# Kernel optimization log

Measured on AMD Instinct MI355X. Metric: run time of the kernel, lower is better.

Reference implementation:

```python
import jax, jax.numpy as jnp
import numpy as np

N_NODES = 100000
N_EDGES = 3200000
IN_F = 256
OUT_F = 128


def setup_inputs() -> dict:
    key = jax.random.key(0)
    k1, k2, k3, k4, k5, k6 = jax.random.split(key, 6)
    x = jax.random.normal(k1, (N_NODES, IN_F), dtype=jnp.float32)
    edge_row = jax.random.randint(k2, (N_EDGES,), 0, N_NODES, dtype=jnp.int32)
    edge_col = jax.random.randint(k3, (N_EDGES,), 0, N_NODES, dtype=jnp.int32)
    edge_val = jax.random.uniform(k4, (N_EDGES,), dtype=jnp.float32)
    # xavier_uniform with relu gain, as in reset_parameters
    gain = float(np.sqrt(2.0))
    bound = gain * float(np.sqrt(6.0 / (IN_F + OUT_F)))
    w = jax.random.uniform(k5, (IN_F, OUT_F), minval=-bound, maxval=bound, dtype=jnp.float32)
    std = 1.0 / float(np.sqrt(OUT_F))
    bias = jax.random.uniform(k6, (OUT_F,), minval=-std, maxval=std, dtype=jnp.float32)
    return {"x": x, "edge_row": edge_row, "edge_col": edge_col,
            "edge_val": edge_val, "w": w, "bias": bias}


def reference(x, edge_row, edge_col, edge_val, w, bias):
    # h = x @ w : dense feature transform [N, out]
    h = jnp.matmul(x, w)
    # spmm(adj, h): out[r] = sum_e adj_val[e] * h[c[e]] for edges e with row r
    msgs = edge_val[:, None] * h[edge_col]  # [E, out]
    agg = jax.ops.segment_sum(msgs, edge_row, num_segments=N_NODES)
    return agg + bias
```

## Files before the change

kernel.cpp:

```cpp
#include <hip/hip_runtime.h>

#define N_NODES 100000
#define N_EDGES 3200000
#define IN_F 256
#define OUT_F 128

#define NBIN 391
#define NBC  512
#define CHUNK 6272
#define GEMM_BLOCKS 782

typedef __attribute__((ext_vector_type(8))) short bf16x8;
typedef __attribute__((ext_vector_type(4))) float f32x4;

union U4BF { uint4 u; bf16x8 v; };

__device__ inline unsigned short f2bf(float f) {
    union { float f; unsigned u; } v; v.f = f;
    unsigned r = v.u + 0x7FFFu + ((v.u >> 16) & 1u);
    return (unsigned short)(r >> 16);
}
__device__ inline unsigned pk2(float a, float b) {
    return (unsigned)f2bf(a) | ((unsigned)f2bf(b) << 16);
}

__global__ __launch_bounds__(256) void conv_w_kernel(
    const float* __restrict__ w, uint4* __restrict__ wbfF)
{
    int tid = blockIdx.x * 256 + threadIdx.x;
    int ks = tid >> 9;
    int fn = (tid >> 6) & 7;
    int l  = tid & 63;
    int c  = fn * 16 + (l & 15);
    int k0 = ks * 32 + (l >> 4) * 8;
    const float* wp = w + (size_t)k0 * OUT_F + c;
    uint4 u;
    u.x = pk2(wp[0 * OUT_F], wp[1 * OUT_F]);
    u.y = pk2(wp[2 * OUT_F], wp[3 * OUT_F]);
    u.z = pk2(wp[4 * OUT_F], wp[5 * OUT_F]);
    u.w = pk2(wp[6 * OUT_F], wp[7 * OUT_F]);
    wbfF[tid] = u;
}

__global__ __launch_bounds__(256) void gemm_hist_kernel(
    const float* __restrict__ x, const uint4* __restrict__ wbfF,
    unsigned short* __restrict__ h,
    const int* __restrict__ erow, int* __restrict__ cntmat)
{
    __shared__ __align__(16) char smem[65536];
    const int t = threadIdx.x;

    if (blockIdx.x < GEMM_BLOCKS) {
        uint4* bsh = (uint4*)smem;
        const int lane = t & 63;
        const int wid  = t >> 6;
        const int brow = blockIdx.x * 128;
        const int ln   = lane & 15;
        const int kb   = lane >> 4;

#pragma unroll
        for (int i = 0; i < 16; ++i) bsh[i * 256 + t] = wbfF[i * 256 + t];

        int r0 = brow + wid * 32 + ln;
        int r1 = r0 + 16;
        const float* a0p = x + (size_t)(r0 < N_NODES ? r0 : N_NODES - 1) * IN_F;
        const float* a1p = x + (size_t)(r1 < N_NODES ? r1 : N_NODES - 1) * IN_F;

        f32x4 acc[2][8] = {};
        __syncthreads();

#pragma unroll
        for (int ks = 0; ks < 8; ++ks) {
            const int k = ks * 32 + kb * 8;
            U4BF a0, a1;
            {
                float4 p = *(const float4*)(a0p + k);
                float4 q = *(const float4*)(a0p + k + 4);
                a0.u.x = pk2(p.x, p.y); a0.u.y = pk2(p.z, p.w);
                a0.u.z = pk2(q.x, q.y); a0.u.w = pk2(q.z, q.w);
            }
            {
                float4 p = *(const float4*)(a1p + k);
                float4 q = *(const float4*)(a1p + k + 4);
                a1.u.x = pk2(p.x, p.y); a1.u.y = pk2(p.z, p.w);
                a1.u.z = pk2(q.x, q.y); a1.u.w = pk2(q.z, q.w);
            }
            U4BF b[8];
#pragma unroll
            for (int fn = 0; fn < 8; ++fn)
                b[fn].u = bsh[(ks * 8 + fn) * 64 + lane];
#pragma unroll
            for (int fn = 0; fn < 8; ++fn) {
                acc[0][fn] = __builtin_amdgcn_mfma_f32_16x16x32_bf16(
                    a0.v, b[fn].v, acc[0][fn], 0, 0, 0);
                acc[1][fn] = __builtin_amdgcn_mfma_f32_16x16x32_bf16(
                    a1.v, b[fn].v, acc[1][fn], 0, 0, 0);
            }
        }

#pragma unroll
        for (int fm = 0; fm < 2; ++fm) {
#pragma unroll
            for (int r = 0; r < 4; ++r) {
                int grow = brow + wid * 32 + fm * 16 + (lane >> 4) * 4 + r;
                if (grow < N_NODES) {
                    unsigned short* dst = h + (size_t)grow * OUT_F + ln;
#pragma unroll
                    for (int fn = 0; fn < 8; ++fn)
                        dst[fn * 16] = f2bf(acc[fm][fn][r]);
                }
            }
        }
    } else {
        int* lhist = (int*)smem;
        const int b = blockIdx.x - GEMM_BLOCKS;
        for (int i = t; i < NBIN; i += 256) lhist[i] = 0;
        __syncthreads();

        const int base = b * CHUNK;
        const int end  = min(base + CHUNK, N_EDGES);
        for (int i = base + t * 4; i < end; i += 1024) {
            int4 r = *(const int4*)(erow + i);
            atomicAdd(&lhist[r.x >> 8], 1);
            atomicAdd(&lhist[r.y >> 8], 1);
            atomicAdd(&lhist[r.z >> 8], 1);
            atomicAdd(&lhist[r.w >> 8], 1);
        }
        __syncthreads();

        int* dst = cntmat + (size_t)b * NBIN;
        for (int j = t; j < NBIN; j += 256) dst[j] = lhist[j];
    }
}

__global__ __launch_bounds__(256) void pass_b_kernel(
    const int* __restrict__ cntmat, int* __restrict__ blockbase,
    int* __restrict__ tot)
{
    __shared__ int sh[256];
    const int t = threadIdx.x;
    const int j = blockIdx.x;
    const int b0 = 2 * t, b1 = 2 * t + 1;
    int c0 = cntmat[(size_t)b0 * NBIN + j];
    int c1 = cntmat[(size_t)b1 * NBIN + j];
    int ps = c0 + c1;
    sh[t] = ps;
    __syncthreads();
    for (int off = 1; off < 256; off <<= 1) {
        int add = (t >= off) ? sh[t - off] : 0;
        __syncthreads();
        sh[t] += add;
        __syncthreads();
    }
    int excl = sh[t] - ps;
    blockbase[(size_t)b0 * NBIN + j] = excl;
    blockbase[(size_t)b1 * NBIN + j] = excl + c0;
    if (t == 255) tot[j] = sh[255];
}

__global__ __launch_bounds__(512) void pass_b2_kernel(
    const int* __restrict__ tot, int* __restrict__ bucket_base)
{
    __shared__ int sh[512];
    const int t = threadIdx.x;
    int v = (t < NBIN) ? tot[t] : 0;
    sh[t] = v;
    __syncthreads();
    for (int off = 1; off < 512; off <<= 1) {
        int add = (t >= off) ? sh[t - off] : 0;
        __syncthreads();
        sh[t] += add;
        __syncthreads();
    }
    if (t < NBIN + 1) bucket_base[t] = sh[t] - v;
}

__global__ __launch_bounds__(256) void pass_c_kernel(
    const int* __restrict__ erow, const int* __restrict__ ecol,
    const float* __restrict__ eval_, const int* __restrict__ blockbase,
    const int* __restrict__ bucket_base, int2* __restrict__ tmp)
{
    __shared__ int cur[NBIN];
    const int t = threadIdx.x;
    const int b = blockIdx.x;
    for (int j = t; j < NBIN; j += 256)
        cur[j] = bucket_base[j] + blockbase[(size_t)b * NBIN + j];
    __syncthreads();

    const int base = b * CHUNK;
    const int end  = min(base + CHUNK, N_EDGES);
    for (int i = base + t * 4; i < end; i += 1024) {
        int4   r = *(const int4*)(erow + i);
        int4   c = *(const int4*)(ecol + i);
        float4 v = *(const float4*)(eval_ + i);
        int p0 = atomicAdd(&cur[r.x >> 8], 1);
        tmp[p0] = make_int2(c.x | ((r.x & 255) << 17), __float_as_int(v.x));
        int p1 = atomicAdd(&cur[r.y >> 8], 1);
        tmp[p1] = make_int2(c.y | ((r.y & 255) << 17), __float_as_int(v.y));
        int p2 = atomicAdd(&cur[r.z >> 8], 1);
        tmp[p2] = make_int2(c.z | ((r.z & 255) << 17), __float_as_int(v.z));
        int p3 = atomicAdd(&cur[r.w >> 8], 1);
        tmp[p3] = make_int2(c.w | ((r.w & 255) << 17), __float_as_int(v.w));
    }
}

__global__ __launch_bounds__(256) void pass_d_kernel(
    const int2* __restrict__ tmp, const int* __restrict__ bucket_base,
    int2* __restrict__ packed, int* __restrict__ row_start,
    int* __restrict__ rowtot)
{
    __shared__ int hist[256];
    __shared__ int cursor[256];
    const int t = threadIdx.x;
    const int j = blockIdx.x;
    const int base = bucket_base[j];
    const int end  = bucket_base[j + 1];

    hist[t] = 0;
    __syncthreads();

    for (int i = base + t; i < end; i += 256)
        atomicAdd(&hist[tmp[i].x >> 17], 1);
    __syncthreads();

    int hv = hist[t];
    cursor[t] = hv;
    __syncthreads();
    for (int off = 1; off < 256; off <<= 1) {
        int add = (t >= off) ? cursor[t - off] : 0;
        __syncthreads();
        cursor[t] += add;
        __syncthreads();
    }
    int excl = cursor[t] - hv;

    int r = j * 256 + t;
    if (r < N_NODES) {
        row_start[r] = base + excl;
        rowtot[r]    = hv;
    }
    __syncthreads();
    cursor[t] = excl;
    __syncthreads();

    for (int i = base + t; i < end; i += 256) {
        int2 p = tmp[i];
        int rl = p.x >> 17;
        int pos = atomicAdd(&cursor[rl], 1);
        packed[base + pos] = make_int2(p.x & 0x1FFFF, p.y);
    }
}

__global__ __launch_bounds__(256) void aggregate_kernel(
    const int2* __restrict__ packed, const int* __restrict__ row_start,
    const int* __restrict__ rowtot, const unsigned* __restrict__ h2,
    const float* __restrict__ bias, float* __restrict__ out)
{
    int wave = (blockIdx.x * 256 + threadIdx.x) >> 6;
    int lane = threadIdx.x & 63;
    if (wave >= N_NODES) return;

    int start = __builtin_amdgcn_readfirstlane(row_start[wave]);
    int deg   = __builtin_amdgcn_readfirstlane(rowtot[wave]);
    int end   = start + deg;

    const unsigned* hb = h2 + lane;
    float ax = 0.f, ay = 0.f;

    int e = start;
    for (; e + 7 < end; e += 8) {
        int2 p0 = packed[e];
        int2 p1 = packed[e + 1];
        int2 p2 = packed[e + 2];
        int2 p3 = packed[e + 3];
        int2 p4 = packed[e + 4];
        int2 p5 = packed[e + 5];
        int2 p6 = packed[e + 6];
        int2 p7 = packed[e + 7];
        unsigned u0 = hb[(size_t)p0.x << 6];
        unsigned u1 = hb[(size_t)p1.x << 6];
        unsigned u2 = hb[(size_t)p2.x << 6];
        unsigned u3 = hb[(size_t)p3.x << 6];
        unsigned u4 = hb[(size_t)p4.x << 6];
        unsigned u5 = hb[(size_t)p5.x << 6];
        unsigned u6 = hb[(size_t)p6.x << 6];
        unsigned u7 = hb[(size_t)p7.x << 6];
        float v0 = __int_as_float(p0.y), v1 = __int_as_float(p1.y);
        float v2 = __int_as_float(p2.y), v3 = __int_as_float(p3.y);
        float v4 = __int_as_float(p4.y), v5 = __int_as_float(p5.y);
        float v6 = __int_as_float(p6.y), v7 = __int_as_float(p7.y);
        ax = fmaf(v0, __uint_as_float(u0 << 16), ax);
        ay = fmaf(v0, __uint_as_float(u0 & 0xFFFF0000u), ay);
        ax = fmaf(v1, __uint_as_float(u1 << 16), ax);
        ay = fmaf(v1, __uint_as_float(u1 & 0xFFFF0000u), ay);
        ax = fmaf(v2, __uint_as_float(u2 << 16), ax);
        ay = fmaf(v2, __uint_as_float(u2 & 0xFFFF0000u), ay);
        ax = fmaf(v3, __uint_as_float(u3 << 16), ax);
        ay = fmaf(v3, __uint_as_float(u3 & 0xFFFF0000u), ay);
        ax = fmaf(v4, __uint_as_float(u4 << 16), ax);
        ay = fmaf(v4, __uint_as_float(u4 & 0xFFFF0000u), ay);
        ax = fmaf(v5, __uint_as_float(u5 << 16), ax);
        ay = fmaf(v5, __uint_as_float(u5 & 0xFFFF0000u), ay);
        ax = fmaf(v6, __uint_as_float(u6 << 16), ax);
        ay = fmaf(v6, __uint_as_float(u6 & 0xFFFF0000u), ay);
        ax = fmaf(v7, __uint_as_float(u7 << 16), ax);
        ay = fmaf(v7, __uint_as_float(u7 & 0xFFFF0000u), ay);
    }
    for (; e < end; ++e) {
        int2 p0 = packed[e];
        unsigned u0 = hb[(size_t)p0.x << 6];
        float v0 = __int_as_float(p0.y);
        ax = fmaf(v0, __uint_as_float(u0 << 16), ax);
        ay = fmaf(v0, __uint_as_float(u0 & 0xFFFF0000u), ay);
    }

    float2 b = *(const float2*)(bias + lane * 2);
    *(float2*)(out + (size_t)wave * OUT_F + lane * 2) = make_float2(ax + b.x, ay + b.y);
}

extern "C" void kernel_launch(void* const* d_in, const int* in_sizes, int n_in,
                              void* d_out, int out_size, void* d_ws, size_t ws_size,
                              hipStream_t stream)
{
    const float* x     = (const float*)d_in[0];
    const int*   erow  = (const int*)d_in[1];
    const int*   ecol  = (const int*)d_in[2];
    const float* eval_ = (const float*)d_in[3];
    const float* w     = (const float*)d_in[4];
    const float* bias  = (const float*)d_in[5];
    float*       out   = (float*)d_out;

    char* ws = (char*)d_ws;
    unsigned short* h           = (unsigned short*)(ws);
    int2*           tmp         = (int2*)(ws + 25600000);
    int2*           packed      = (int2*)(ws + 51200000);
    int*            cntmat      = (int*)(ws + 76800000);
    int*            blockbase   = (int*)(ws + 77600768);
    int*            tot         = (int*)(ws + 78401536);
    int*            bucket_base = (int*)(ws + 78403104);
    int*            row_start   = (int*)(ws + 78404672);
    int*            rowtot      = (int*)(ws + 78804672);
    uint4*          wbfF        = (uint4*)(ws + 79204672);

    hipLaunchKernelGGL(conv_w_kernel, dim3(16), dim3(256), 0, stream, w, wbfF);

    hipLaunchKernelGGL(gemm_hist_kernel, dim3(GEMM_BLOCKS + NBC), dim3(256), 0, stream,
                       x, wbfF, h, erow, cntmat);

    hipLaunchKernelGGL(pass_b_kernel, dim3(NBIN), dim3(256), 0, stream,
                       cntmat, blockbase, tot);
    hipLaunchKernelGGL(pass_b2_kernel, dim3(1), dim3(512), 0, stream, tot, bucket_base);

    hipLaunchKernelGGL(pass_c_kernel, dim3(NBC), dim3(256), 0, stream,
                       erow, ecol, eval_, blockbase, bucket_base, tmp);

    hipLaunchKernelGGL(pass_d_kernel, dim3(NBIN), dim3(256), 0, stream,
                       tmp, bucket_base, packed, row_start, rowtot);

    hipLaunchKernelGGL(aggregate_kernel,
                       dim3((N_NODES * 64 + 255) / 256), dim3(256), 0, stream,
                       packed, row_start, rowtot, (const unsigned*)h, bias, out);
}
```

Measured before the change: 237.2 us.

## Stage bucket scatter in shared memory for coalesced writes in pass_c

pass_c now sorts each chunk's edges by bucket in LDS, using a local prefix scan over the per-block counts, and then writes them to the global temp buffer in contiguous runs. The old version scattered each edge straight to a random global slot. The number of partition blocks grows from 512 to 800 with smaller chunks so the LDS staging (about 48KB) fits, and pass_b now scans four counts per thread to match. The bf16 conversion also switches to the HIP intrinsic. The costs are an extra shared-memory pass and lower occupancy from the large LDS use.

```diff
diff --git a/kernel.cpp b/kernel.cpp
--- a/kernel.cpp
+++ b/kernel.cpp
@@ -1,4 +1,5 @@
 #include <hip/hip_runtime.h>
+#include <hip/hip_bf16.h>
 
 #define N_NODES 100000
 #define N_EDGES 3200000
@@ -6,8 +7,8 @@
 #define OUT_F 128
 
 #define NBIN 391
-#define NBC  512
-#define CHUNK 6272
+#define NBC  800
+#define CHUNK 4000
 #define GEMM_BLOCKS 782
 
 typedef __attribute__((ext_vector_type(8))) short bf16x8;
@@ -16,12 +17,12 @@
 union U4BF { uint4 u; bf16x8 v; };
 
 __device__ inline unsigned short f2bf(float f) {
-    union { float f; unsigned u; } v; v.f = f;
-    unsigned r = v.u + 0x7FFFu + ((v.u >> 16) & 1u);
-    return (unsigned short)(r >> 16);
+    return __bfloat16_as_ushort(__float2bfloat16(f));
 }
 __device__ inline unsigned pk2(float a, float b) {
-    return (unsigned)f2bf(a) | ((unsigned)f2bf(b) << 16);
+    unsigned la = __bfloat16_as_ushort(__float2bfloat16(a));
+    unsigned lb = __bfloat16_as_ushort(__float2bfloat16(b));
+    return la | (lb << 16);
 }
 
 __global__ __launch_bounds__(256) void conv_w_kernel(
@@ -140,10 +141,14 @@
     __shared__ int sh[256];
     const int t = threadIdx.x;
     const int j = blockIdx.x;
-    const int b0 = 2 * t, b1 = 2 * t + 1;
-    int c0 = cntmat[(size_t)b0 * NBIN + j];
-    int c1 = cntmat[(size_t)b1 * NBIN + j];
-    int ps = c0 + c1;
+    int c[4];
+    int ps = 0;
+#pragma unroll
+    for (int i = 0; i < 4; ++i) {
+        int bb = 4 * t + i;
+        c[i] = (bb < NBC) ? cntmat[(size_t)bb * NBIN + j] : 0;
+        ps += c[i];
+    }
     sh[t] = ps;
     __syncthreads();
     for (int off = 1; off < 256; off <<= 1) {
@@ -153,8 +158,11 @@
         __syncthreads();
     }
     int excl = sh[t] - ps;
-    blockbase[(size_t)b0 * NBIN + j] = excl;
-    blockbase[(size_t)b1 * NBIN + j] = excl + c0;
+#pragma unroll
+    for (int i = 0; i < 4; ++i) {
+        int bb = 4 * t + i;
+        if (bb < NBC) { blockbase[(size_t)bb * NBIN + j] = excl; excl += c[i]; }
+    }
     if (t == 255) tot[j] = sh[255];
 }
 
@@ -177,14 +185,40 @@
 
 __global__ __launch_bounds__(256) void pass_c_kernel(
     const int* __restrict__ erow, const int* __restrict__ ecol,
-    const float* __restrict__ eval_, const int* __restrict__ blockbase,
-    const int* __restrict__ bucket_base, int2* __restrict__ tmp)
-{
-    __shared__ int cur[NBIN];
+    const float* __restrict__ eval_, const int* __restrict__ cntmat,
+    const int* __restrict__ blockbase, const int* __restrict__ bucket_base,
+    int2* __restrict__ tmp)
+{
+    __shared__ int2 skv[CHUNK];
+    __shared__ int  sdelta[CHUNK];
+    __shared__ int  cur[NBIN];
+    __shared__ int  sdel[NBIN];
+    __shared__ int  sscan[256];
+
     const int t = threadIdx.x;
     const int b = blockIdx.x;
-    for (int j = t; j < NBIN; j += 256)
-        cur[j] = bucket_base[j] + blockbase[(size_t)b * NBIN + j];
+
+    int j0 = 2 * t, j1 = 2 * t + 1;
+    int c0 = (j0 < NBIN) ? cntmat[(size_t)b * NBIN + j0] : 0;
+    int c1 = (j1 < NBIN) ? cntmat[(size_t)b * NBIN + j1] : 0;
+    int ps = c0 + c1;
+    sscan[t] = ps;
+    __syncthreads();
+    for (int off = 1; off < 256; off <<= 1) {
+        int add = (t >= off) ? sscan[t - off] : 0;
+        __syncthreads();
+        sscan[t] += add;
+        __syncthreads();
+    }
+    int excl = sscan[t] - ps;
+    if (j0 < NBIN) {
+        cur[j0]  = excl;
+        sdel[j0] = bucket_base[j0] + blockbase[(size_t)b * NBIN + j0] - excl;
+    }
+    if (j1 < NBIN) {
+        cur[j1]  = excl + c0;
+        sdel[j1] = bucket_base[j1] + blockbase[(size_t)b * NBIN + j1] - (excl + c0);
+    }
     __syncthreads();
 
     const int base = b * CHUNK;
@@ -193,14 +227,26 @@
         int4   r = *(const int4*)(erow + i);
         int4   c = *(const int4*)(ecol + i);
         float4 v = *(const float4*)(eval_ + i);
-        int p0 = atomicAdd(&cur[r.x >> 8], 1);
-        tmp[p0] = make_int2(c.x | ((r.x & 255) << 17), __float_as_int(v.x));
-        int p1 = atomicAdd(&cur[r.y >> 8], 1);
-        tmp[p1] = make_int2(c.y | ((r.y & 255) << 17), __float_as_int(v.y));
-        int p2 = atomicAdd(&cur[r.z >> 8], 1);
-        tmp[p2] = make_int2(c.z | ((r.z & 255) << 17), __float_as_int(v.z));
-        int p3 = atomicAdd(&cur[r.w >> 8], 1);
-        tmp[p3] = make_int2(c.w | ((r.w & 255) << 17), __float_as_int(v.w));
+        int bin, pos;
+        bin = r.x >> 8; pos = atomicAdd(&cur[bin], 1);
+        skv[pos] = make_int2(c.x | ((r.x & 255) << 17), __float_as_int(v.x));
+        sdelta[pos] = sdel[bin];
+        bin = r.y >> 8; pos = atomicAdd(&cur[bin], 1);
+        skv[pos] = make_int2(c.y | ((r.y & 255) << 17), __float_as_int(v.y));
+        sdelta[pos] = sdel[bin];
+        bin = r.z >> 8; pos = atomicAdd(&cur[bin], 1);
+        skv[pos] = make_int2(c.z | ((r.z & 255) << 17), __float_as_int(v.z));
+        sdelta[pos] = sdel[bin];
+        bin = r.w >> 8; pos = atomicAdd(&cur[bin], 1);
+        skv[pos] = make_int2(c.w | ((r.w & 255) << 17), __float_as_int(v.w));
+        sdelta[pos] = sdel[bin];
+    }
+    __syncthreads();
+
+    const int n = end - base;
+    for (int i = t; i < n; i += 256) {
+        int2 kv = skv[i];
+        tmp[sdelta[i] + i] = kv;
     }
 }
 
@@ -335,12 +381,12 @@
     int2*           tmp         = (int2*)(ws + 25600000);
     int2*           packed      = (int2*)(ws + 51200000);
     int*            cntmat      = (int*)(ws + 76800000);
-    int*            blockbase   = (int*)(ws + 77600768);
-    int*            tot         = (int*)(ws + 78401536);
-    int*            bucket_base = (int*)(ws + 78403104);
-    int*            row_start   = (int*)(ws + 78404672);
-    int*            rowtot      = (int*)(ws + 78804672);
-    uint4*          wbfF        = (uint4*)(ws + 79204672);
+    int*            blockbase   = (int*)(ws + 78051200);
+    int*            tot         = (int*)(ws + 79302400);
+    int*            bucket_base = (int*)(ws + 79303968);
+    int*            row_start   = (int*)(ws + 79305536);
+    int*            rowtot      = (int*)(ws + 79705536);
+    uint4*          wbfF        = (uint4*)(ws + 80105536);
 
     hipLaunchKernelGGL(conv_w_kernel, dim3(16), dim3(256), 0, stream, w, wbfF);
 
@@ -352,7 +398,7 @@
     hipLaunchKernelGGL(pass_b2_kernel, dim3(1), dim3(512), 0, stream, tot, bucket_base);
 
     hipLaunchKernelGGL(pass_c_kernel, dim3(NBC), dim3(256), 0, stream,
-                       erow, ecol, eval_, blockbase, bucket_base, tmp);
+                       erow, ecol, eval_, cntmat, blockbase, bucket_base, tmp);
 
     hipLaunchKernelGGL(pass_d_kernel, dim3(NBIN), dim3(256), 0, stream,
                        tmp, bucket_base, packed, row_start, rowtot);
```

Result: faster. 216.9 us (-8.6%).
